# Kernel tuning notes

Hardware: AMD Instinct MI355X
Metric: run time of the kernel (lower is better)

## Reference

```python
import jax, jax.numpy as jnp
import numpy as np

MAX_REL = 8  # max_relative_position
B, H, L, D = 2, 16, 2048, 64


def setup_inputs() -> dict:
    key = jax.random.key(0)
    kq, kk, kv, kb = jax.random.split(key, 4)
    return {
        "q": jax.random.normal(kq, (B, H, L, D), dtype=jnp.float32),
        "k": jax.random.normal(kk, (B, H, L, D), dtype=jnp.float32),
        "v": jax.random.normal(kv, (B, H, L, D), dtype=jnp.float32),
        "relative_bias": jax.random.normal(kb, (2 * MAX_REL + 1,), dtype=jnp.float32),
    }


def reference(q, k, v, relative_bias):
    Bq, Hq, Lq, Dq = q.shape
    scale = jnp.sqrt(jnp.asarray(Dq, dtype=q.dtype))
    # [B,H,L,L] attention scores
    scores = jnp.einsum("bhqd,bhkd->bhqk", q, k) / scale
    pos = jnp.arange(Lq)
    rel = pos[None, :] - pos[:, None]                 # [L,L] (col - row), matches torch code
    idx = jnp.clip(rel, -MAX_REL, MAX_REL) + MAX_REL  # [L,L] in [0, 2*MAX_REL]
    bias = relative_bias[idx]                         # [L,L] gather from bias table
    scores = scores + bias[None, None, :, :]
    attn = jax.nn.softmax(scores, axis=-1)
    return jnp.einsum("bhqk,bhkd->bhqd", attn, v)
```

## Files before the change

kernel.cpp:

```cpp
#include <hip/hip_runtime.h>
#include <hip/hip_bf16.h>


#define LOG2E 1.44269504088896f

constexpr int Lv = 2048, Dv = 64;
constexpr int BH  = 32;
constexpr int BQ  = 128;
constexpr int BKT = 64;
constexpr int NQT = Lv / BQ;
constexpr int NKT = Lv / BKT;
constexpr int LDK = 72;
constexpr int LDO = 68;
constexpr int MAXREL = 8;

typedef __bf16 bf16x8 __attribute__((ext_vector_type(8)));
typedef __bf16 bf16x4 __attribute__((ext_vector_type(4)));
typedef float  f32x4  __attribute__((ext_vector_type(4)));

static __device__ __forceinline__ unsigned pack2bf(float a, float b) {
    __bf16 x = (__bf16)a, y = (__bf16)b;
    unsigned short ux = __builtin_bit_cast(unsigned short, x);
    unsigned short uy = __builtin_bit_cast(unsigned short, y);
    return (unsigned)ux | ((unsigned)uy << 16);
}

__global__
__attribute__((amdgpu_flat_work_group_size(512, 512), amdgpu_waves_per_eu(4, 4)))
void relattn_kernel(
    const float* __restrict__ Q, const float* __restrict__ K,
    const float* __restrict__ V, const float* __restrict__ RB,
    float* __restrict__ O)
{
    constexpr int SKBYTES  = 2 * BKT * LDK * 2;
    constexpr int SVBYTES  = 2 * Dv  * LDK * 2;
    constexpr int PADBYTES = 20480;
    __shared__ __align__(16) unsigned char smem[SKBYTES + SVBYTES + PADBYTES];
    __shared__ float sRB[2 * MAXREL + 1];
    __bf16* sK = (__bf16*)smem;
    __bf16* sV = (__bf16*)(smem + SKBYTES);

    const int tid  = threadIdx.x;
    const int w    = tid >> 6;
    const int lane = tid & 63;
    const int l16  = lane & 15;
    const int lg   = lane >> 4;
    const int pair = w >> 1;
    const int wh   = w & 1;

    const int bh = blockIdx.x & (BH - 1);
    const int qt = blockIdx.x >> 5;

    const size_t base = (size_t)bh * Lv * Dv;
    const float* Qb = Q + base + (size_t)qt * BQ * Dv;
    const float* Kb = K + base;
    const float* Vb = V + base;
    float*       Ob = O + base + (size_t)qt * BQ * Dv;

    if (tid < 2 * MAXREL + 1) sRB[tid] = RB[tid] * LOG2E;

    const float qsc = 0.125f * LOG2E;
    bf16x8 qfrag[2][2];
    #pragma unroll
    for (int h = 0; h < 2; ++h) {
        const float* qrow = Qb + (pair * 32 + h * 16 + l16) * Dv;
        #pragma unroll
        for (int s = 0; s < 2; ++s) {
            const float4 a = *(const float4*)(qrow + lg * 8 + 32 * s);
            const float4 b = *(const float4*)(qrow + lg * 8 + 32 * s + 4);
            bf16x8 f;
            f[0] = (__bf16)(a.x * qsc); f[1] = (__bf16)(a.y * qsc);
            f[2] = (__bf16)(a.z * qsc); f[3] = (__bf16)(a.w * qsc);
            f[4] = (__bf16)(b.x * qsc); f[5] = (__bf16)(b.y * qsc);
            f[6] = (__bf16)(b.z * qsc); f[7] = (__bf16)(b.w * qsc);
            qfrag[h][s] = f;
        }
    }

    f32x4 oacc[2][4];
    float lacc[2][2];
    #pragma unroll
    for (int h = 0; h < 2; ++h) {
        lacc[h][0] = 0.f; lacc[h][1] = 0.f;
        #pragma unroll
        for (int t = 0; t < 4; ++t)
            #pragma unroll
            for (int r = 0; r < 4; ++r) oacc[h][t][r] = 0.f;
    }

    const int kr0 = tid >> 4;
    const int kc4 = (tid & 15) * 4;
    const int vkk0 = (tid & 31) * 2;
    const int vd0  = (tid >> 5) * 4;
    const int vcol = (vkk0 & 35) | ((vkk0 & 12) << 1) | ((vkk0 & 16) >> 2);

    float4 kreg[2], vreg[2];
    bf16x4   kpk[2];
    unsigned vpk[4];

    auto loadKV = [&](int kt) {
        const float* Ks = Kb + (size_t)kt * BKT * Dv;
        const float* Vs = Vb + (size_t)kt * BKT * Dv;
        kreg[0] = *(const float4*)(Ks + kr0 * Dv + kc4);
        kreg[1] = *(const float4*)(Ks + (32 + kr0) * Dv + kc4);
        vreg[0] = *(const float4*)(Vs + vkk0 * Dv + vd0);
        vreg[1] = *(const float4*)(Vs + (vkk0 + 1) * Dv + vd0);
    };
    auto convKV = [&]() {
        #pragma unroll
        for (int p = 0; p < 2; ++p) {
            bf16x4 pk;
            pk[0] = (__bf16)kreg[p].x; pk[1] = (__bf16)kreg[p].y;
            pk[2] = (__bf16)kreg[p].z; pk[3] = (__bf16)kreg[p].w;
            kpk[p] = pk;
        }
        #pragma unroll
        for (int j = 0; j < 4; ++j)
            vpk[j] = pack2bf(vreg[0][j], vreg[1][j]);
    };

    loadKV(0);
    convKV();

    const int qw0 = qt * BQ + pair * 32;
    const int qgl = qw0 + l16;

    for (int kt = 0; kt < NKT; ++kt) {
        const int buf = kt & 1;
        __bf16* sKb = sK + buf * (BKT * LDK);
        __bf16* sVb = sV + buf * (Dv * LDK);

        *(bf16x4*)&sKb[kr0 * LDK + kc4]          = kpk[0];
        *(bf16x4*)&sKb[(32 + kr0) * LDK + kc4]   = kpk[1];
        #pragma unroll
        for (int j = 0; j < 4; ++j)
            *(unsigned*)&sVb[(vd0 + j) * LDK + vcol] = vpk[j];
        if (kt + 1 < NKT) loadKV(kt + 1);
        __syncthreads();

        f32x4 sacc[2][2];
        #pragma unroll
        for (int h = 0; h < 2; ++h)
            #pragma unroll
            for (int tl = 0; tl < 2; ++tl)
                #pragma unroll
                for (int r = 0; r < 4; ++r) sacc[h][tl][r] = 0.f;
        #pragma unroll
        for (int s = 0; s < 2; ++s) {
            #pragma unroll
            for (int tl = 0; tl < 2; ++tl) {
                bf16x8 a = *(const bf16x8*)&sKb[((2 * wh + tl) * 16 + l16) * LDK + lg * 8 + 32 * s];
                sacc[0][tl] = __builtin_amdgcn_mfma_f32_16x16x32_bf16(a, qfrag[0][s], sacc[0][tl], 0, 0, 0);
                sacc[1][tl] = __builtin_amdgcn_mfma_f32_16x16x32_bf16(a, qfrag[1][s], sacc[1][tl], 0, 0, 0);
            }
        }

        if (kt + 1 < NKT) convKV();

        const int k0 = kt * BKT + wh * 32;
        bf16x8 pfrag[2];
        #pragma unroll
        for (int h = 0; h < 2; ++h) {
            const int qlo = qw0 + h * 16;
            if (k0 >= qlo + 15 + MAXREL) {
                const float bc = sRB[2 * MAXREL];
                #pragma unroll
                for (int tl = 0; tl < 2; ++tl)
                    #pragma unroll
                    for (int r = 0; r < 4; ++r) {
                        float p = __builtin_amdgcn_exp2f(sacc[h][tl][r] + bc);
                        lacc[h][r & 1] += p;
                        pfrag[h][tl * 4 + r] = (__bf16)p;
                    }
            } else if (k0 + 31 + MAXREL <= qlo) {
                const float bc = sRB[0];
                #pragma unroll
                for (int tl = 0; tl < 2; ++tl)
                    #pragma unroll
                    for (int r = 0; r < 4; ++r) {
                        float p = __builtin_amdgcn_exp2f(sacc[h][tl][r] + bc);
                        lacc[h][r & 1] += p;
                        pfrag[h][tl * 4 + r] = (__bf16)p;
                    }
            } else {
                const int kkb = k0 + lg * 4 - (qgl + h * 16);
                #pragma unroll
                for (int tl = 0; tl < 2; ++tl) {
                    #pragma unroll
                    for (int r = 0; r < 4; ++r) {
                        int d = kkb + tl * 16 + r;
                        d = d < -MAXREL ? -MAXREL : (d > MAXREL ? MAXREL : d);
                        float p = __builtin_amdgcn_exp2f(sacc[h][tl][r] + sRB[d + MAXREL]);
                        lacc[h][r & 1] += p;
                        pfrag[h][tl * 4 + r] = (__bf16)p;
                    }
                }
            }
        }

        #pragma unroll
        for (int t = 0; t < 4; ++t) {
            bf16x8 vf = *(const bf16x8*)&sVb[(t * 16 + l16) * LDK + lg * 8 + 32 * wh];
            oacc[0][t] = __builtin_amdgcn_mfma_f32_16x16x32_bf16(vf, pfrag[0], oacc[0][t], 0, 0, 0);
            oacc[1][t] = __builtin_amdgcn_mfma_f32_16x16x32_bf16(vf, pfrag[1], oacc[1][t], 0, 0, 0);
        }
    }

    float lh[2];
    #pragma unroll
    for (int h = 0; h < 2; ++h) {
        float l = lacc[h][0] + lacc[h][1];
        l += __shfl_xor(l, 16);
        l += __shfl_xor(l, 32);
        lh[h] = l;
    }

    __syncthreads();
    float* sO = (float*)smem;
    float* sL = (float*)(smem + 4 * 32 * LDO * 4);
    if (wh == 1) {
        #pragma unroll
        for (int h = 0; h < 2; ++h) {
            #pragma unroll
            for (int t = 0; t < 4; ++t)
                *(f32x4*)&sO[(pair * 32 + h * 16 + l16) * LDO + t * 16 + lg * 4] = oacc[h][t];
            if (lg == 0) sL[pair * 32 + h * 16 + l16] = lh[h];
        }
    }
    __syncthreads();
    if (wh == 0) {
        #pragma unroll
        for (int h = 0; h < 2; ++h) {
            const float lt = lh[h] + sL[pair * 32 + h * 16 + l16];
            const float linv = 1.f / lt;
            float* orow = Ob + (pair * 32 + h * 16 + l16) * Dv;
            #pragma unroll
            for (int t = 0; t < 4; ++t) {
                f32x4 oo = *(const f32x4*)&sO[(pair * 32 + h * 16 + l16) * LDO + t * 16 + lg * 4];
                float4 o;
                o.x = (oacc[h][t][0] + oo[0]) * linv;
                o.y = (oacc[h][t][1] + oo[1]) * linv;
                o.z = (oacc[h][t][2] + oo[2]) * linv;
                o.w = (oacc[h][t][3] + oo[3]) * linv;
                *(float4*)(orow + t * 16 + lg * 4) = o;
            }
        }
    }
}

extern "C" void kernel_launch(void* const* d_in, const int* in_sizes, int n_in,
                              void* d_out, int out_size, void* d_ws, size_t ws_size,
                              hipStream_t stream) {
    const float* q  = (const float*)d_in[0];
    const float* k  = (const float*)d_in[1];
    const float* v  = (const float*)d_in[2];
    const float* rb = (const float*)d_in[3];
    float* out = (float*)d_out;
    relattn_kernel<<<dim3(BH * NQT), dim3(512), 0, stream>>>(q, k, v, rb, out);
}
```

Before: 136.6 us.

## Fold relative bias into MFMA accumulator init and compute row sums via MFMA

The score accumulators are now initialised with the relative-position bias, so the bias add after QK^T goes away and exp2 is applied directly to the MFMA output. The per-lane softmax denominator adds and the cross-lane shuffle reduction are replaced by an extra MFMA per row group that multiplies a ones vector by the bf16 probability fragment. This moves VALU work onto the matrix unit. In exchange it adds two MFMAs per tile, and the row sums are now taken from bf16-rounded probabilities, which stays consistent with the PV product.

Measured after the change: 136.9 us. No clear change (+0.2%).

```diff
diff --git a/kernel.cpp b/kernel.cpp
--- a/kernel.cpp
+++ b/kernel.cpp
@@ -77,11 +77,16 @@
         }
     }
 
+    bf16x8 ones;
+    #pragma unroll
+    for (int j = 0; j < 8; ++j) ones[j] = (__bf16)1.0f;
+
     f32x4 oacc[2][4];
-    float lacc[2][2];
+    f32x4 lfrag[2];
     #pragma unroll
     for (int h = 0; h < 2; ++h) {
-        lacc[h][0] = 0.f; lacc[h][1] = 0.f;
+        #pragma unroll
+        for (int r = 0; r < 4; ++r) lfrag[h][r] = 0.f;
         #pragma unroll
         for (int t = 0; t < 4; ++t)
             #pragma unroll
@@ -138,13 +143,37 @@
         if (kt + 1 < NKT) loadKV(kt + 1);
         __syncthreads();
 
+        const int k0 = kt * BKT + wh * 32;
         f32x4 sacc[2][2];
         #pragma unroll
-        for (int h = 0; h < 2; ++h)
-            #pragma unroll
-            for (int tl = 0; tl < 2; ++tl)
-                #pragma unroll
-                for (int r = 0; r < 4; ++r) sacc[h][tl][r] = 0.f;
+        for (int h = 0; h < 2; ++h) {
+            const int qlo = qw0 + h * 16;
+            if (k0 >= qlo + 15 + MAXREL) {
+                const float bc = sRB[2 * MAXREL];
+                #pragma unroll
+                for (int tl = 0; tl < 2; ++tl)
+                    #pragma unroll
+                    for (int r = 0; r < 4; ++r) sacc[h][tl][r] = bc;
+            } else if (k0 + 31 + MAXREL <= qlo) {
+                const float bc = sRB[0];
+                #pragma unroll
+                for (int tl = 0; tl < 2; ++tl)
+                    #pragma unroll
+                    for (int r = 0; r < 4; ++r) sacc[h][tl][r] = bc;
+            } else {
+                const int kkb = k0 + lg * 4 - (qgl + h * 16);
+                #pragma unroll
+                for (int tl = 0; tl < 2; ++tl) {
+                    #pragma unroll
+                    for (int r = 0; r < 4; ++r) {
+                        int d = kkb + tl * 16 + r;
+                        d = d < -MAXREL ? -MAXREL : (d > MAXREL ? MAXREL : d);
+                        sacc[h][tl][r] = sRB[d + MAXREL];
+                    }
+                }
+            }
+        }
+
         #pragma unroll
         for (int s = 0; s < 2; ++s) {
             #pragma unroll
@@ -157,46 +186,18 @@
 
         if (kt + 1 < NKT) convKV();
 
-        const int k0 = kt * BKT + wh * 32;
         bf16x8 pfrag[2];
         #pragma unroll
-        for (int h = 0; h < 2; ++h) {
-            const int qlo = qw0 + h * 16;
-            if (k0 >= qlo + 15 + MAXREL) {
-                const float bc = sRB[2 * MAXREL];
-                #pragma unroll
-                for (int tl = 0; tl < 2; ++tl)
-                    #pragma unroll
-                    for (int r = 0; r < 4; ++r) {
-                        float p = __builtin_amdgcn_exp2f(sacc[h][tl][r] + bc);
-                        lacc[h][r & 1] += p;
-                        pfrag[h][tl * 4 + r] = (__bf16)p;
-                    }
-            } else if (k0 + 31 + MAXREL <= qlo) {
-                const float bc = sRB[0];
-                #pragma unroll
-                for (int tl = 0; tl < 2; ++tl)
-                    #pragma unroll
-                    for (int r = 0; r < 4; ++r) {
-                        float p = __builtin_amdgcn_exp2f(sacc[h][tl][r] + bc);
-                        lacc[h][r & 1] += p;
-                        pfrag[h][tl * 4 + r] = (__bf16)p;
-                    }
-            } else {
-                const int kkb = k0 + lg * 4 - (qgl + h * 16);
-                #pragma unroll
-                for (int tl = 0; tl < 2; ++tl) {
-                    #pragma unroll
-                    for (int r = 0; r < 4; ++r) {
-                        int d = kkb + tl * 16 + r;
-                        d = d < -MAXREL ? -MAXREL : (d > MAXREL ? MAXREL : d);
-                        float p = __builtin_amdgcn_exp2f(sacc[h][tl][r] + sRB[d + MAXREL]);
-                        lacc[h][r & 1] += p;
-                        pfrag[h][tl * 4 + r] = (__bf16)p;
-                    }
-                }
-            }
-        }
+        for (int h = 0; h < 2; ++h)
+            #pragma unroll
+            for (int tl = 0; tl < 2; ++tl)
+                #pragma unroll
+                for (int r = 0; r < 4; ++r)
+                    pfrag[h][tl * 4 + r] =
+                        (__bf16)__builtin_amdgcn_exp2f(sacc[h][tl][r]);
+
+        lfrag[0] = __builtin_amdgcn_mfma_f32_16x16x32_bf16(ones, pfrag[0], lfrag[0], 0, 0, 0);
+        lfrag[1] = __builtin_amdgcn_mfma_f32_16x16x32_bf16(ones, pfrag[1], lfrag[1], 0, 0, 0);
 
         #pragma unroll
         for (int t = 0; t < 4; ++t) {
@@ -207,13 +208,8 @@
     }
 
     float lh[2];
-    #pragma unroll
-    for (int h = 0; h < 2; ++h) {
-        float l = lacc[h][0] + lacc[h][1];
-        l += __shfl_xor(l, 16);
-        l += __shfl_xor(l, 32);
-        lh[h] = l;
-    }
+    lh[0] = lfrag[0][0];
+    lh[1] = lfrag[1][0];
 
     __syncthreads();
     float* sO = (float*)smem;
```
